# Optimization experiments

Measured on AMD Instinct MI355X. Metric: run time of the kernel, lower is better.

## Reference

```python
import jax, jax.numpy as jnp
import numpy as np

NUM_LATENTS = 8192
LATENT_DIM = 256


def setup_inputs() -> dict:
    key = jax.random.key(0)
    kx, kw = jax.random.split(key)
    x = jax.random.normal(kx, (32, 512, LATENT_DIM), dtype=jnp.float32)
    # codebook init: uniform(-1/K, 1/K), matching nn.Embedding init in the module
    bound = 1.0 / NUM_LATENTS
    codebook = jax.random.uniform(
        kw, (NUM_LATENTS, LATENT_DIM), dtype=jnp.float32, minval=-bound, maxval=bound
    )
    return {"x": x, "codebook": codebook}


def reference(x, codebook):
    # torch.cdist(x, W) followed by argmin. Since sqrt is monotone, argmin over
    # squared Euclidean distance gives identical indices; we expand
    x2 = jnp.sum(x * x, axis=-1, keepdims=True)              # [B, T, 1]
    w2 = jnp.sum(codebook * codebook, axis=-1)               # [K]
    xw = jnp.einsum("btd,kd->btk", x, codebook)              # [B, T, K]
    dist2 = x2 - 2.0 * xw + w2                               # [B, T, K]
    indices = jnp.argmin(dist2, axis=-1)                     # [B, T] int
    z = codebook[indices]                                    # [B, T, D]
    # straight-through estimator: z_q = x + stop_grad(z - x)
    z_q = x + jax.lax.stop_gradient(z - x)
    return (z_q, z, x, indices)
```

## Files before the change

### kernel.cpp

```cpp
#include <hip/hip_runtime.h>
#include <hip/hip_bf16.h>
#include <cstddef>
#include <cstdint>

#define M_TOK   16384
#define N_CODE  8192
#define K_DIM   256
#define NSPLIT  4
#define BM      128
#define BN      128
#define BK      64


typedef short bf16x8 __attribute__((ext_vector_type(8)));
typedef float f32x4  __attribute__((ext_vector_type(4)));

__device__ __forceinline__ unsigned short f2bf_rne(float f) {
    unsigned u = __float_as_uint(f);
    unsigned r = u + 0x7FFFu + ((u >> 16) & 1u);
    return (unsigned short)(r >> 16);
}
__device__ __forceinline__ float bf2f(unsigned short h) {
    union { unsigned u; float f; } c; c.u = ((unsigned)h) << 16; return c.f;
}

__device__ __forceinline__ void gload16(const void* g, void* l) {
    __builtin_amdgcn_global_load_lds(
        (const __attribute__((address_space(1))) void*)g,
        (__attribute__((address_space(3))) void*)l, 16, 0, 0);
}

__global__ void vq_prep(const float* __restrict__ x, const float* __restrict__ cb,
                        unsigned short* __restrict__ xh, unsigned short* __restrict__ xl,
                        unsigned short* __restrict__ wh, unsigned short* __restrict__ wl,
                        float* __restrict__ x2, float* __restrict__ w2) {
    int gt   = blockIdx.x * blockDim.x + threadIdx.x;
    int row  = gt >> 6;
    int lane = gt & 63;
    if (row >= M_TOK + N_CODE) return;
    const float* src; unsigned short *dh, *dl; float* dn;
    if (row < M_TOK) {
        src = x + (size_t)row * K_DIM;
        dh = xh + (size_t)row * K_DIM; dl = xl + (size_t)row * K_DIM; dn = x2 + row;
    } else {
        int r = row - M_TOK;
        src = cb + (size_t)r * K_DIM;
        dh = wh + (size_t)r * K_DIM; dl = wl + (size_t)r * K_DIM; dn = w2 + r;
    }
    float4 v = ((const float4*)src)[lane];
    unsigned short h0 = f2bf_rne(v.x), h1 = f2bf_rne(v.y);
    unsigned short h2 = f2bf_rne(v.z), h3 = f2bf_rne(v.w);
    unsigned short l0 = f2bf_rne(v.x - bf2f(h0)), l1 = f2bf_rne(v.y - bf2f(h1));
    unsigned short l2 = f2bf_rne(v.z - bf2f(h2)), l3 = f2bf_rne(v.w - bf2f(h3));
    ushort4 hv; hv.x = h0; hv.y = h1; hv.z = h2; hv.w = h3;
    ushort4 lv; lv.x = l0; lv.y = l1; lv.z = l2; lv.w = l3;
    ((ushort4*)dh)[lane] = hv;
    ((ushort4*)dl)[lane] = lv;
    float s = v.x*v.x + v.y*v.y + v.z*v.z + v.w*v.w;
    #pragma unroll
    for (int off = 32; off > 0; off >>= 1) s += __shfl_down(s, off);
    if (lane == 0) *dn = s;
}

__global__ __launch_bounds__(256, 2)
void vq_main_mfma(const unsigned short* __restrict__ xh, const unsigned short* __restrict__ xl,
                  const unsigned short* __restrict__ wh, const unsigned short* __restrict__ wl,
                  const float* __restrict__ x2, const float* __restrict__ w2,
                  float* __restrict__ pminv, int* __restrict__ pmini) {
    __shared__ unsigned short xh_s[BM][BK];
    __shared__ unsigned short xl_s[BM][BK];
    __shared__ unsigned short wh_s[BN][BK];
    __shared__ unsigned short wl_s[BN][BK];
    __shared__ float red_d[BM][2];
    __shared__ int   red_i[BM][2];

    const int split = blockIdx.x;
    const int mtile = blockIdx.y;
    const int gm    = mtile * BM;
    const int tid   = threadIdx.x;
    const int w     = tid >> 6;
    const int lane  = tid & 63;
    const int wr    = w >> 1;
    const int wc    = w & 1;
    const int quad  = lane >> 4;
    const int l15   = lane & 15;

    const int w32   = w * 32;
    const int srl   = lane >> 3;
    const int sg    = (lane & 7) ^ srl;

    float x2r[16];
    #pragma unroll
    for (int rt = 0; rt < 4; ++rt)
        #pragma unroll
        for (int reg = 0; reg < 4; ++reg)
            x2r[rt*4+reg] = x2[gm + wr*64 + rt*16 + quad*4 + reg];

    float minv[16];
    int   mini[16];
    #pragma unroll
    for (int i = 0; i < 16; ++i) { minv[i] = 3.4e38f; mini[i] = 0; }

    const char* xhp = (const char*)xh;
    const char* xlp = (const char*)xl;
    const char* whp = (const char*)wh;
    const char* wlp = (const char*)wl;

    const int tiles = (N_CODE / NSPLIT) / BN;
    for (int tile = 0; tile < tiles; ++tile) {
        const int nb = split * (N_CODE / NSPLIT) + tile * BN;

        f32x4 acc[4][4];
        #pragma unroll
        for (int rt = 0; rt < 4; ++rt)
            #pragma unroll
            for (int ct = 0; ct < 4; ++ct)
                acc[rt][ct] = (f32x4){0.f, 0.f, 0.f, 0.f};

        for (int kc = 0; kc < K_DIM / BK; ++kc) {
            __syncthreads();
            #pragma unroll
            for (int i = 0; i < 4; ++i) {
                int rowl = w32 + i * 8 + srl;
                size_t xoff = (size_t)(gm + rowl) * (K_DIM*2) + kc*(BK*2) + sg*16;
                size_t woff = (size_t)(nb + rowl) * (K_DIM*2) + kc*(BK*2) + sg*16;
                unsigned ldso = (unsigned)w32 * (BK*2) + i * 1024;
                gload16(xhp + xoff, (char*)&xh_s[0][0] + ldso);
                gload16(xlp + xoff, (char*)&xl_s[0][0] + ldso);
                gload16(whp + woff, (char*)&wh_s[0][0] + ldso);
                gload16(wlp + woff, (char*)&wl_s[0][0] + ldso);
            }
            __syncthreads();

            #pragma unroll
            for (int ks = 0; ks < 2; ++ks) {
                bf16x8 ah[4], al[4], bh[4], bl[4];
                const int sl = ((ks << 2) + quad) ^ (l15 & 7);
                #pragma unroll
                for (int rt = 0; rt < 4; ++rt) {
                    int off = (wr*64 + rt*16 + l15) * (BK*2) + sl*16;
                    ah[rt] = *(const bf16x8*)((const char*)&xh_s[0][0] + off);
                    al[rt] = *(const bf16x8*)((const char*)&xl_s[0][0] + off);
                }
                #pragma unroll
                for (int ct = 0; ct < 4; ++ct) {
                    int off = (wc*64 + ct*16 + l15) * (BK*2) + sl*16;
                    bh[ct] = *(const bf16x8*)((const char*)&wh_s[0][0] + off);
                    bl[ct] = *(const bf16x8*)((const char*)&wl_s[0][0] + off);
                }
                #pragma unroll
                for (int rt = 0; rt < 4; ++rt)
                    #pragma unroll
                    for (int ct = 0; ct < 4; ++ct) {
                        acc[rt][ct] = __builtin_amdgcn_mfma_f32_16x16x32_bf16(al[rt], bh[ct], acc[rt][ct], 0, 0, 0);
                        acc[rt][ct] = __builtin_amdgcn_mfma_f32_16x16x32_bf16(ah[rt], bl[ct], acc[rt][ct], 0, 0, 0);
                        acc[rt][ct] = __builtin_amdgcn_mfma_f32_16x16x32_bf16(ah[rt], bh[ct], acc[rt][ct], 0, 0, 0);
                    }
            }
        }

        float w2c[4];
        int   cidx[4];
        #pragma unroll
        for (int ct = 0; ct < 4; ++ct) {
            cidx[ct] = nb + wc*64 + ct*16 + l15;
            w2c[ct]  = w2[cidx[ct]];
        }
        #pragma unroll
        for (int rt = 0; rt < 4; ++rt)
            #pragma unroll
            for (int ct = 0; ct < 4; ++ct) {
                #pragma unroll
                for (int reg = 0; reg < 4; ++reg) {
                    float d = (x2r[rt*4+reg] - 2.0f * acc[rt][ct][reg]) + w2c[ct];
                    int r16 = rt*4 + reg;
                    if (d < minv[r16]) { minv[r16] = d; mini[r16] = cidx[ct]; }
                }
            }
    }

    #pragma unroll
    for (int r16 = 0; r16 < 16; ++r16) {
        float d  = minv[r16];
        int   ix = mini[r16];
        #pragma unroll
        for (int off = 1; off < 16; off <<= 1) {
            float od = __shfl_xor(d, off);
            int   oi = __shfl_xor(ix, off);
            if (od < d || (od == d && oi < ix)) { d = od; ix = oi; }
        }
        if (l15 == 0) {
            int row_local = wr*64 + (r16 >> 2)*16 + quad*4 + (r16 & 3);
            red_d[row_local][wc] = d;
            red_i[row_local][wc] = ix;
        }
    }
    __syncthreads();
    if (tid < BM) {
        float d0 = red_d[tid][0], d1 = red_d[tid][1];
        int   i0 = red_i[tid][0], i1 = red_i[tid][1];
        float d; int ix;
        if (d1 < d0 || (d1 == d0 && i1 < i0)) { d = d1; ix = i1; } else { d = d0; ix = i0; }
        pminv[(size_t)(gm + tid) * NSPLIT + split] = d;
        pmini[(size_t)(gm + tid) * NSPLIT + split] = ix;
    }
}

__global__ void vq_gather(const float* __restrict__ x, const float* __restrict__ cb,
                          const float* __restrict__ pminv, const int* __restrict__ pmini,
                          float* __restrict__ out) {
    int t = blockIdx.x * blockDim.x + threadIdx.x;
    int m = t >> 6;
    int q = t & 63;

    float d  = pminv[(size_t)m * NSPLIT + (q & (NSPLIT-1))];
    int   ix = pmini[(size_t)m * NSPLIT + (q & (NSPLIT-1))];
    #pragma unroll
    for (int off = 1; off < NSPLIT; off <<= 1) {
        float od = __shfl_xor(d, off);
        int   oi = __shfl_xor(ix, off);
        if (od < d || (od == d && oi < ix)) { d = od; ix = oi; }
    }

    float4 xv = ((const float4*)x)[t];
    float4 zv = ((const float4*)cb)[(size_t)ix * 64 + q];
    float4 zq;
    zq.x = xv.x + (zv.x - xv.x);
    zq.y = xv.y + (zv.y - xv.y);
    zq.z = xv.z + (zv.z - xv.z);
    zq.w = xv.w + (zv.w - xv.w);
    float4* o = (float4*)out;
    const int ELEM4 = M_TOK * 64;
    o[t]           = zq;
    o[t + ELEM4]   = zv;
    o[t + 2*ELEM4] = xv;
    if (q == 0) out[(size_t)3 * M_TOK * K_DIM + m] = (float)ix;
}

extern "C" void kernel_launch(void* const* d_in, const int* in_sizes, int n_in,
                              void* d_out, int out_size, void* d_ws, size_t ws_size,
                              hipStream_t stream) {
    const float* x  = (const float*)d_in[0];
    const float* cb = (const float*)d_in[1];
    float* out = (float*)d_out;

    char* p = (char*)d_ws;
    unsigned short* xh = (unsigned short*)p;  p += (size_t)M_TOK  * K_DIM * 2;
    unsigned short* xl = (unsigned short*)p;  p += (size_t)M_TOK  * K_DIM * 2;
    unsigned short* wh = (unsigned short*)p;  p += (size_t)N_CODE * K_DIM * 2;
    unsigned short* wl = (unsigned short*)p;  p += (size_t)N_CODE * K_DIM * 2;
    float* x2    = (float*)p;  p += (size_t)M_TOK * 4;
    float* w2    = (float*)p;  p += (size_t)N_CODE * 4;
    float* pminv = (float*)p;  p += (size_t)M_TOK * NSPLIT * 4;
    int*   pmini = (int*)p;    p += (size_t)M_TOK * NSPLIT * 4;

    {
        int waves = M_TOK + N_CODE;
        vq_prep<<<(waves * 64 + 255) / 256, 256, 0, stream>>>(x, cb, xh, xl, wh, wl, x2, w2);
    }
    {
        dim3 grid(NSPLIT, M_TOK / BM);
        vq_main_mfma<<<grid, 256, 0, stream>>>(xh, xl, wh, wl, x2, w2, pminv, pmini);
    }
    {
        int t = M_TOK * (K_DIM / 4);
        vq_gather<<<t / 256, 256, 0, stream>>>(x, cb, pminv, pmini, out);
    }
}
```

Baseline: 281.9 us.

## Switch distance GEMM from 16x16x32 to 32x32x16 bf16 MFMA tiles

```diff
diff --git a/kernel.cpp b/kernel.cpp
--- a/kernel.cpp
+++ b/kernel.cpp
@@ -14,6 +14,7 @@
 
 typedef short bf16x8 __attribute__((ext_vector_type(8)));
 typedef float f32x4  __attribute__((ext_vector_type(4)));
+typedef float f32x16 __attribute__((ext_vector_type(16)));
 
 __device__ __forceinline__ unsigned short f2bf_rne(float f) {
     unsigned u = __float_as_uint(f);
@@ -82,24 +83,17 @@
     const int lane  = tid & 63;
     const int wr    = w >> 1;
     const int wc    = w & 1;
-    const int quad  = lane >> 4;
-    const int l15   = lane & 15;
+    const int l31   = lane & 31;
+    const int hi    = lane >> 5;
 
     const int w32   = w * 32;
     const int srl   = lane >> 3;
     const int sg    = (lane & 7) ^ srl;
 
-    float x2r[16];
-    #pragma unroll
-    for (int rt = 0; rt < 4; ++rt)
-        #pragma unroll
-        for (int reg = 0; reg < 4; ++reg)
-            x2r[rt*4+reg] = x2[gm + wr*64 + rt*16 + quad*4 + reg];
-
-    float minv[16];
-    int   mini[16];
-    #pragma unroll
-    for (int i = 0; i < 16; ++i) { minv[i] = 3.4e38f; mini[i] = 0; }
+    float minv[32];
+    int   mini[32];
+    #pragma unroll
+    for (int i = 0; i < 32; ++i) { minv[i] = 3.4e38f; mini[i] = 0; }
 
     const char* xhp = (const char*)xh;
     const char* xlp = (const char*)xl;
@@ -110,12 +104,14 @@
     for (int tile = 0; tile < tiles; ++tile) {
         const int nb = split * (N_CODE / NSPLIT) + tile * BN;
 
-        f32x4 acc[4][4];
-        #pragma unroll
-        for (int rt = 0; rt < 4; ++rt)
-            #pragma unroll
-            for (int ct = 0; ct < 4; ++ct)
-                acc[rt][ct] = (f32x4){0.f, 0.f, 0.f, 0.f};
+        f32x16 acc[2][2];
+        #pragma unroll
+        for (int rt = 0; rt < 2; ++rt)
+            #pragma unroll
+            for (int ct = 0; ct < 2; ++ct)
+                #pragma unroll
+                for (int r = 0; r < 16; ++r)
+                    acc[rt][ct][r] = 0.f;
 
         for (int kc = 0; kc < K_DIM / BK; ++kc) {
             __syncthreads();
@@ -133,64 +129,71 @@
             __syncthreads();
 
             #pragma unroll
-            for (int ks = 0; ks < 2; ++ks) {
-                bf16x8 ah[4], al[4], bh[4], bl[4];
-                const int sl = ((ks << 2) + quad) ^ (l15 & 7);
-                #pragma unroll
-                for (int rt = 0; rt < 4; ++rt) {
-                    int off = (wr*64 + rt*16 + l15) * (BK*2) + sl*16;
+            for (int ks = 0; ks < 4; ++ks) {
+                const int sl = ((ks << 1) + hi) ^ (lane & 7);
+                bf16x8 ah[2], al[2], bh[2], bl[2];
+                #pragma unroll
+                for (int rt = 0; rt < 2; ++rt) {
+                    int off = (wr*64 + rt*32 + l31) * (BK*2) + sl*16;
                     ah[rt] = *(const bf16x8*)((const char*)&xh_s[0][0] + off);
                     al[rt] = *(const bf16x8*)((const char*)&xl_s[0][0] + off);
                 }
                 #pragma unroll
-                for (int ct = 0; ct < 4; ++ct) {
-                    int off = (wc*64 + ct*16 + l15) * (BK*2) + sl*16;
+                for (int ct = 0; ct < 2; ++ct) {
+                    int off = (wc*64 + ct*32 + l31) * (BK*2) + sl*16;
                     bh[ct] = *(const bf16x8*)((const char*)&wh_s[0][0] + off);
                     bl[ct] = *(const bf16x8*)((const char*)&wl_s[0][0] + off);
                 }
                 #pragma unroll
-                for (int rt = 0; rt < 4; ++rt)
+                for (int rt = 0; rt < 2; ++rt)
                     #pragma unroll
-                    for (int ct = 0; ct < 4; ++ct) {
-                        acc[rt][ct] = __builtin_amdgcn_mfma_f32_16x16x32_bf16(al[rt], bh[ct], acc[rt][ct], 0, 0, 0);
-                        acc[rt][ct] = __builtin_amdgcn_mfma_f32_16x16x32_bf16(ah[rt], bl[ct], acc[rt][ct], 0, 0, 0);
-                        acc[rt][ct] = __builtin_amdgcn_mfma_f32_16x16x32_bf16(ah[rt], bh[ct], acc[rt][ct], 0, 0, 0);
+                    for (int ct = 0; ct < 2; ++ct) {
+                        acc[rt][ct] = __builtin_amdgcn_mfma_f32_32x32x16_bf16(al[rt], bh[ct], acc[rt][ct], 0, 0, 0);
+                        acc[rt][ct] = __builtin_amdgcn_mfma_f32_32x32x16_bf16(ah[rt], bl[ct], acc[rt][ct], 0, 0, 0);
+                        acc[rt][ct] = __builtin_amdgcn_mfma_f32_32x32x16_bf16(ah[rt], bh[ct], acc[rt][ct], 0, 0, 0);
                     }
             }
         }
 
-        float w2c[4];
-        int   cidx[4];
-        #pragma unroll
-        for (int ct = 0; ct < 4; ++ct) {
-            cidx[ct] = nb + wc*64 + ct*16 + l15;
+        f32x4 x2v[2][4];
+        #pragma unroll
+        for (int rt = 0; rt < 2; ++rt)
+            #pragma unroll
+            for (int rq = 0; rq < 4; ++rq)
+                x2v[rt][rq] = *(const f32x4*)(x2 + gm + wr*64 + rt*32 + 4*hi + rq*8);
+        float w2c[2];
+        int   cidx[2];
+        #pragma unroll
+        for (int ct = 0; ct < 2; ++ct) {
+            cidx[ct] = nb + wc*64 + ct*32 + l31;
             w2c[ct]  = w2[cidx[ct]];
         }
         #pragma unroll
-        for (int rt = 0; rt < 4; ++rt)
-            #pragma unroll
-            for (int ct = 0; ct < 4; ++ct) {
-                #pragma unroll
-                for (int reg = 0; reg < 4; ++reg) {
-                    float d = (x2r[rt*4+reg] - 2.0f * acc[rt][ct][reg]) + w2c[ct];
-                    int r16 = rt*4 + reg;
-                    if (d < minv[r16]) { minv[r16] = d; mini[r16] = cidx[ct]; }
+        for (int rt = 0; rt < 2; ++rt)
+            #pragma unroll
+            for (int ct = 0; ct < 2; ++ct) {
+                #pragma unroll
+                for (int r = 0; r < 16; ++r) {
+                    float d = (x2v[rt][r >> 2][r & 3] - 2.0f * acc[rt][ct][r]) + w2c[ct];
+                    int s = rt*16 + r;
+                    if (d < minv[s]) { minv[s] = d; mini[s] = cidx[ct]; }
                 }
             }
     }
 
     #pragma unroll
-    for (int r16 = 0; r16 < 16; ++r16) {
-        float d  = minv[r16];
-        int   ix = mini[r16];
-        #pragma unroll
-        for (int off = 1; off < 16; off <<= 1) {
+    for (int s = 0; s < 32; ++s) {
+        float d  = minv[s];
+        int   ix = mini[s];
+        #pragma unroll
+        for (int off = 1; off < 32; off <<= 1) {
             float od = __shfl_xor(d, off);
             int   oi = __shfl_xor(ix, off);
             if (od < d || (od == d && oi < ix)) { d = od; ix = oi; }
         }
-        if (l15 == 0) {
-            int row_local = wr*64 + (r16 >> 2)*16 + quad*4 + (r16 & 3);
+        if (l31 == 0) {
+            int rt = s >> 4, r = s & 15;
+            int row_local = wr*64 + rt*32 + 4*hi + (r & 3) + 8*(r >> 2);
             red_d[row_local][wc] = d;
             red_i[row_local][wc] = ix;
         }
```

Result: slower. 325.8 us (+15.6%).
